# Optimization experiments

Hardware: AMD Instinct MI355X
Metric: run time of the kernel (lower is better)

The kernel has to match this reference:

```python
import jax, jax.numpy as jnp
import numpy as np

MODES = 256


def setup_inputs() -> dict:
    key = jax.random.key(0)
    k1, k2, k3, k4, k5 = jax.random.split(key, 5)
    B, C_IN, C_OUT, N, KM = 8, 128, 128, 8192, 32
    scale = 1.0 / (C_IN * C_OUT)
    return {
        "x": jax.random.normal(k1, (B, C_IN, N), dtype=jnp.float32),
        "wbases": jax.random.normal(k2, (B, N, MODES), dtype=jnp.float32),
        "bases": jax.random.normal(k3, (B, N, MODES), dtype=jnp.float32),
        "weights": scale * jax.random.normal(k4, (C_IN, C_OUT, KM), dtype=jnp.float32),
        "D": jax.random.normal(k5, (KM, MODES), dtype=jnp.float32),
    }


def reference(x, wbases, bases, weights, D):
    # Project onto weighted bases: (b, c_in, n) x (b, n, modes) -> (b, c_in, modes)
    x_hat = jnp.einsum('bcx,bxk->bck', x, wbases[:, :, :MODES])
    # D-weighted channel mixing. Original: x_hat1[b,i,j,k] = x_hat[b,i,k]*D[j,k];
    # y[b,o,k] = sum_{i,j} x_hat1[b,i,j,k] * weights[i,o,j]
    # Equivalent fused contraction (same math, no 4D broadcast):
    y_hat = jnp.einsum('bik,jk,ioj->bok', x_hat, D, weights)
    # Reconstruct on output bases: (b, c_out, modes) x (b, n, modes) -> (b, c_out, n)
    y = jnp.einsum('bck,bxk->bcx', y_hat, bases[:, :, :MODES])
    return y
```

## Files before the change

### kernel.cpp

```cpp
#include <hip/hip_runtime.h>

#define B_    8
#define CIN   128
#define COUT  128
#define NX    8192
#define KMJ   32
#define MODES 256

typedef short bf16x8 __attribute__((ext_vector_type(8)));
typedef float f32x4  __attribute__((ext_vector_type(4)));

__device__ __forceinline__ float bf2f(unsigned short u) {
    union { unsigned int i; float f; } v; v.i = ((unsigned int)u) << 16; return v.f;
}
__device__ __forceinline__ unsigned short f2bf(float f) {
    union { float f; unsigned int i; } v; v.f = f;
    unsigned int x = v.i;
    return (unsigned short)((x + 0x7fffu + ((x >> 16) & 1u)) >> 16);
}
__device__ __forceinline__ bf16x8 cvt8(const float* __restrict__ p) {
    f32x4 a = *(const f32x4*)p;
    f32x4 b = *(const f32x4*)(p + 4);
    bf16x8 r;
    r[0] = (short)f2bf(a[0]); r[1] = (short)f2bf(a[1]);
    r[2] = (short)f2bf(a[2]); r[3] = (short)f2bf(a[3]);
    r[4] = (short)f2bf(b[0]); r[5] = (short)f2bf(b[1]);
    r[6] = (short)f2bf(b[2]); r[7] = (short)f2bf(b[3]);
    return r;
}
__device__ __forceinline__ ushort4 cvt4(f32x4 a) {
    ushort4 r;
    r.x = f2bf(a[0]); r.y = f2bf(a[1]); r.z = f2bf(a[2]); r.w = f2bf(a[3]);
    return r;
}

__global__ __launch_bounds__(256) void k1_wk(const float* __restrict__ W,
                                             const float* __restrict__ D,
                                             unsigned short* __restrict__ Wk) {
    int wave = threadIdx.x >> 6;
    int lane = threadIdx.x & 63;
    int gw   = blockIdx.x * 4 + wave;
    int kt   = gw & 15;
    int ioch = gw >> 4;
    int k0   = kt * 16;
    int quad = lane >> 4, l16 = lane & 15;

    bf16x8 bfrag;
#pragma unroll
    for (int jj = 0; jj < 8; jj++)
        bfrag[jj] = (short)f2bf(D[(quad * 8 + jj) * MODES + k0 + l16]);

    int io0 = ioch * 256;
#pragma unroll 4
    for (int t = 0; t < 16; t++) {
        int io = io0 + t * 16 + l16;
        bf16x8 afrag = cvt8(W + (size_t)io * KMJ + quad * 8);
        f32x4 acc = {0.f, 0.f, 0.f, 0.f};
        acc = __builtin_amdgcn_mfma_f32_16x16x32_bf16(afrag, bfrag, acc, 0, 0, 0);
        int iorow = io0 + t * 16 + quad * 4;
        ushort4 st;
        st.x = f2bf(acc[0]); st.y = f2bf(acc[1]);
        st.z = f2bf(acc[2]); st.w = f2bf(acc[3]);
        *(ushort4*)(Wk + (size_t)(k0 + l16) * (CIN * COUT) + iorow) = st;
    }
}

__global__ __launch_bounds__(256) void k2_xhat(const float* __restrict__ X,
                                               const float* __restrict__ WB,
                                               float* __restrict__ XH) {
    __shared__ __align__(16) unsigned short Xs[128 * 40];
    __shared__ __align__(16) unsigned short WBs[32 * 140];
    int nt = blockIdx.x;
    int kt = blockIdx.y;
    int b  = blockIdx.z;
    int r0 = nt * 256;
    int t  = threadIdx.x;
    int wave = t >> 6, lane = t & 63;
    int wm = wave >> 1, wn = wave & 1;
    int quad = lane >> 4, l16 = lane & 15;

    const float* xb  = X  + (size_t)b * CIN * NX;
    const float* wbb = WB + (size_t)b * NX * MODES + kt * 128;

    int xn4 = t & 7,  xc0 = t >> 3;
    int wm4 = t & 31, wn0 = t >> 5;

    f32x4 acc[4][4];
#pragma unroll
    for (int i = 0; i < 4; i++)
#pragma unroll
        for (int j = 0; j < 4; j++) acc[i][j] = (f32x4){0.f, 0.f, 0.f, 0.f};

    for (int s = 0; s < 8; s++) {
        int rs = r0 + s * 32;
        f32x4 xv[4], wv[4];
#pragma unroll
        for (int r = 0; r < 4; r++)
            xv[r] = *(const f32x4*)(xb + (size_t)(xc0 + 32 * r) * NX + rs + xn4 * 4);
#pragma unroll
        for (int r = 0; r < 4; r++)
            wv[r] = *(const f32x4*)(wbb + (size_t)(rs + wn0 + 8 * r) * MODES + wm4 * 4);

        __syncthreads();
#pragma unroll
        for (int r = 0; r < 4; r++)
            *(ushort4*)(Xs + (xc0 + 32 * r) * 40 + xn4 * 4) = cvt4(xv[r]);
#pragma unroll
        for (int r = 0; r < 4; r++)
            *(ushort4*)(WBs + (wn0 + 8 * r) * 140 + wm4 * 4) = cvt4(wv[r]);
        __syncthreads();

        bf16x8 af[4];
#pragma unroll
        for (int tm = 0; tm < 4; tm++) {
            int c = wm * 64 + tm * 16 + l16;
            af[tm] = *(const bf16x8*)(Xs + c * 40 + quad * 8);
        }
        bf16x8 bfv[4];
#pragma unroll
        for (int tn = 0; tn < 4; tn++) {
            int km = wn * 64 + tn * 16 + l16;
#pragma unroll
            for (int jj = 0; jj < 8; jj++)
                bfv[tn][jj] = (short)WBs[(quad * 8 + jj) * 140 + km];
        }
#pragma unroll
        for (int tm = 0; tm < 4; tm++)
#pragma unroll
            for (int tn = 0; tn < 4; tn++)
                acc[tm][tn] = __builtin_amdgcn_mfma_f32_16x16x32_bf16(af[tm], bfv[tn], acc[tm][tn], 0, 0, 0);
    }

    float* xhb = XH + (size_t)b * CIN * MODES + kt * 128;
#pragma unroll
    for (int tm = 0; tm < 4; tm++) {
        int c = wm * 64 + tm * 16 + quad * 4;
#pragma unroll
        for (int tn = 0; tn < 4; tn++) {
            int km = wn * 64 + tn * 16 + l16;
#pragma unroll
            for (int r = 0; r < 4; r++)
                atomicAdd(xhb + (size_t)(c + r) * MODES + km, acc[tm][tn][r]);
        }
    }
}

__global__ __launch_bounds__(256) void k3_yhat(const float* __restrict__ XH,
                                               const unsigned short* __restrict__ Wk,
                                               unsigned short* __restrict__ YH) {
    __shared__ float xs[8][128];
    __shared__ float ys[8][128];
    int b  = blockIdx.y;
    int k0 = blockIdx.x * 8;
    int t  = threadIdx.x;
    const float* xhb = XH + (size_t)b * CIN * MODES;
#pragma unroll
    for (int l = 0; l < 4; l++) {
        int e = l * 256 + t;
        int kk = e & 7, i = e >> 3;
        xs[kk][i] = xhb[(size_t)i * MODES + k0 + kk];
    }
    __syncthreads();
    int o = t & 127, kh = t >> 7;
#pragma unroll
    for (int p = 0; p < 4; p++) {
        int kk = p * 2 + kh;
        int k  = k0 + kk;
        const unsigned short* wp = Wk + (size_t)k * (CIN * COUT) + o;
        float acc = 0.f;
#pragma unroll 8
        for (int i = 0; i < 128; i++)
            acc += xs[kk][i] * bf2f(wp[i * COUT]);
        ys[kk][o] = acc;
    }
    __syncthreads();
    unsigned short* yb = YH + (size_t)b * COUT * MODES;
#pragma unroll
    for (int l = 0; l < 4; l++) {
        int e = l * 256 + t;
        int kk = e & 7, oo = e >> 3;
        yb[(size_t)oo * MODES + k0 + kk] = f2bf(ys[kk][oo]);
    }
}

__global__ __launch_bounds__(256) void k4_y(const unsigned short* __restrict__ YH,
                                            const float* __restrict__ BA,
                                            float* __restrict__ Y) {
    __shared__ __align__(16) unsigned short As[128 * 32];
    __shared__ __align__(16) unsigned short Bs[128 * 32];
    int b  = blockIdx.y;
    int n0 = blockIdx.x * 128;
    int t  = threadIdx.x;
    int wave = t >> 6, lane = t & 63;
    int wm = wave >> 1, wn = wave & 1;
    int quad = lane >> 4, l16 = lane & 15;

    const unsigned short* yhb = YH + (size_t)b * COUT * MODES;
    const float* bab = BA + (size_t)b * NX * MODES + (size_t)n0 * MODES;

    f32x4 acc[4][4];
#pragma unroll
    for (int i = 0; i < 4; i++)
#pragma unroll
        for (int j = 0; j < 4; j++) acc[i][j] = (f32x4){0.f, 0.f, 0.f, 0.f};

    for (int step = 0; step < 8; step++) {
        int ks = step * 32;
#pragma unroll
        for (int p = 0; p < 2; p++) {
            int E = p * 2048 + t * 8;
            int row = E >> 5, kk = E & 31;
            bf16x8 av = *(const bf16x8*)(yhb + (size_t)row * MODES + ks + kk);
            bf16x8 bv = cvt8(bab + (size_t)row * MODES + ks + kk);
            *(bf16x8*)(As + E) = av;
            *(bf16x8*)(Bs + E) = bv;
        }
        __syncthreads();

        bf16x8 af[4], bfv[4];
#pragma unroll
        for (int tm = 0; tm < 4; tm++) {
            int c = wm * 64 + tm * 16 + l16;
            af[tm] = *(const bf16x8*)(As + c * 32 + quad * 8);
        }
#pragma unroll
        for (int tn = 0; tn < 4; tn++) {
            int n = wn * 64 + tn * 16 + l16;
            bfv[tn] = *(const bf16x8*)(Bs + n * 32 + quad * 8);
        }
#pragma unroll
        for (int tm = 0; tm < 4; tm++)
#pragma unroll
            for (int tn = 0; tn < 4; tn++)
                acc[tm][tn] = __builtin_amdgcn_mfma_f32_16x16x32_bf16(af[tm], bfv[tn], acc[tm][tn], 0, 0, 0);
        __syncthreads();
    }

    float* yb = Y + (size_t)b * COUT * NX;
#pragma unroll
    for (int tm = 0; tm < 4; tm++) {
        int o = wm * 64 + tm * 16 + quad * 4;
#pragma unroll
        for (int tn = 0; tn < 4; tn++) {
            int n = n0 + wn * 64 + tn * 16 + l16;
#pragma unroll
            for (int r = 0; r < 4; r++)
                yb[(size_t)(o + r) * NX + n] = acc[tm][tn][r];
        }
    }
}

extern "C" void kernel_launch(void* const* d_in, const int* in_sizes, int n_in,
                              void* d_out, int out_size, void* d_ws, size_t ws_size,
                              hipStream_t stream) {
    const float* X  = (const float*)d_in[0];
    const float* WB = (const float*)d_in[1];
    const float* BA = (const float*)d_in[2];
    const float* W  = (const float*)d_in[3];
    const float* D  = (const float*)d_in[4];
    float* Y = (float*)d_out;

    char* ws = (char*)d_ws;
    float*          XH = (float*)ws;
    unsigned short* Wk = (unsigned short*)(ws + (1u << 20));
    unsigned short* YH = (unsigned short*)(ws + (1u << 20) + (size_t)CIN * COUT * MODES * 2);

    hipMemsetAsync(XH, 0, (size_t)B_ * CIN * MODES * sizeof(float), stream);

    k1_wk  <<<256,            256, 0, stream>>>(W, D, Wk);
    k2_xhat<<<dim3(32, 2, 8), 256, 0, stream>>>(X, WB, XH);
    k3_yhat<<<dim3(32, 8),    256, 0, stream>>>(XH, Wk, YH);
    k4_y   <<<dim3(64, 8),    256, 0, stream>>>(YH, BA, Y);
}
```

Measured before the change: 251.1 us.

## Replace atomics with bf16 partials plus reduction, rework Wk layout and prefetch in k4

The x_hat kernel now uses 512-thread blocks covering all 256 modes and writes per-tile bf16 partial sums, which a new reduction kernel sums, replacing the float atomics and the memset. The Wk layout becomes [k][o][i], so k3 processes one mode across all batches with vectorized weight loads. k4 gains register prefetch of the next K-slice to overlap global loads with MFMA. The risks are extra partial-buffer traffic and bf16 rounding of the partial sums.

```diff
diff --git a/kernel.cpp b/kernel.cpp
--- a/kernel.cpp
+++ b/kernel.cpp
@@ -37,53 +37,43 @@
 __global__ __launch_bounds__(256) void k1_wk(const float* __restrict__ W,
                                              const float* __restrict__ D,
                                              unsigned short* __restrict__ Wk) {
-    int wave = threadIdx.x >> 6;
-    int lane = threadIdx.x & 63;
-    int gw   = blockIdx.x * 4 + wave;
-    int kt   = gw & 15;
-    int ioch = gw >> 4;
-    int k0   = kt * 16;
+    int wave = threadIdx.x >> 6, lane = threadIdx.x & 63;
     int quad = lane >> 4, l16 = lane & 15;
-
-    bf16x8 bfrag;
-#pragma unroll
-    for (int jj = 0; jj < 8; jj++)
-        bfrag[jj] = (short)f2bf(D[(quad * 8 + jj) * MODES + k0 + l16]);
-
-    int io0 = ioch * 256;
-#pragma unroll 4
-    for (int t = 0; t < 16; t++) {
-        int io = io0 + t * 16 + l16;
-        bf16x8 afrag = cvt8(W + (size_t)io * KMJ + quad * 8);
+    int gw  = blockIdx.x * 4 + wave;
+    int oi0 = gw * 16;
+    int i0  = oi0 & 127, o0 = oi0 >> 7;
+    bf16x8 bfrag = cvt8(W + ((size_t)(i0 + l16) * COUT + o0) * KMJ + quad * 8);
+    for (int mt = 0; mt < 16; mt++) {
+        int k0 = mt * 16;
+        bf16x8 afrag;
+#pragma unroll
+        for (int jj = 0; jj < 8; jj++)
+            afrag[jj] = (short)f2bf(D[(quad * 8 + jj) * MODES + k0 + l16]);
         f32x4 acc = {0.f, 0.f, 0.f, 0.f};
         acc = __builtin_amdgcn_mfma_f32_16x16x32_bf16(afrag, bfrag, acc, 0, 0, 0);
-        int iorow = io0 + t * 16 + quad * 4;
-        ushort4 st;
-        st.x = f2bf(acc[0]); st.y = f2bf(acc[1]);
-        st.z = f2bf(acc[2]); st.w = f2bf(acc[3]);
-        *(ushort4*)(Wk + (size_t)(k0 + l16) * (CIN * COUT) + iorow) = st;
-    }
-}
-
-__global__ __launch_bounds__(256) void k2_xhat(const float* __restrict__ X,
+#pragma unroll
+        for (int r = 0; r < 4; r++)
+            Wk[(size_t)(k0 + quad * 4 + r) * (CIN * COUT) + oi0 + l16] = f2bf(acc[r]);
+    }
+}
+
+__global__ __launch_bounds__(512) void k2_xhat(const float* __restrict__ X,
                                                const float* __restrict__ WB,
-                                               float* __restrict__ XH) {
+                                               unsigned short* __restrict__ PART) {
     __shared__ __align__(16) unsigned short Xs[128 * 40];
-    __shared__ __align__(16) unsigned short WBs[32 * 140];
-    int nt = blockIdx.x;
-    int kt = blockIdx.y;
-    int b  = blockIdx.z;
+    __shared__ __align__(16) unsigned short WBs[32 * 260];
+    int nt = blockIdx.x, b = blockIdx.y;
     int r0 = nt * 256;
     int t  = threadIdx.x;
     int wave = t >> 6, lane = t & 63;
-    int wm = wave >> 1, wn = wave & 1;
+    int wm = wave >> 2, wn = wave & 3;
     int quad = lane >> 4, l16 = lane & 15;
 
     const float* xb  = X  + (size_t)b * CIN * NX;
-    const float* wbb = WB + (size_t)b * NX * MODES + kt * 128;
-
-    int xn4 = t & 7,  xc0 = t >> 3;
-    int wm4 = t & 31, wn0 = t >> 5;
+    const float* wbb = WB + (size_t)b * NX * MODES;
+
+    int xn4 = t & 7,  xc  = t >> 3;
+    int wk4 = t & 63, wn0 = t >> 6;
 
     f32x4 acc[4][4];
 #pragma unroll
@@ -93,36 +83,32 @@
 
     for (int s = 0; s < 8; s++) {
         int rs = r0 + s * 32;
-        f32x4 xv[4], wv[4];
+        f32x4 xv0 = *(const f32x4*)(xb + (size_t)xc * NX + rs + xn4 * 4);
+        f32x4 xv1 = *(const f32x4*)(xb + (size_t)(xc + 64) * NX + rs + xn4 * 4);
+        f32x4 wv[4];
 #pragma unroll
         for (int r = 0; r < 4; r++)
-            xv[r] = *(const f32x4*)(xb + (size_t)(xc0 + 32 * r) * NX + rs + xn4 * 4);
+            wv[r] = *(const f32x4*)(wbb + (size_t)(rs + wn0 + 8 * r) * MODES + wk4 * 4);
+
+        __syncthreads();
+        *(ushort4*)(Xs + xc * 40 + xn4 * 4)        = cvt4(xv0);
+        *(ushort4*)(Xs + (xc + 64) * 40 + xn4 * 4) = cvt4(xv1);
 #pragma unroll
         for (int r = 0; r < 4; r++)
-            wv[r] = *(const f32x4*)(wbb + (size_t)(rs + wn0 + 8 * r) * MODES + wm4 * 4);
-
-        __syncthreads();
-#pragma unroll
-        for (int r = 0; r < 4; r++)
-            *(ushort4*)(Xs + (xc0 + 32 * r) * 40 + xn4 * 4) = cvt4(xv[r]);
-#pragma unroll
-        for (int r = 0; r < 4; r++)
-            *(ushort4*)(WBs + (wn0 + 8 * r) * 140 + wm4 * 4) = cvt4(wv[r]);
+            *(ushort4*)(WBs + (wn0 + 8 * r) * 260 + wk4 * 4) = cvt4(wv[r]);
         __syncthreads();
 
         bf16x8 af[4];
 #pragma unroll
-        for (int tm = 0; tm < 4; tm++) {
-            int c = wm * 64 + tm * 16 + l16;
-            af[tm] = *(const bf16x8*)(Xs + c * 40 + quad * 8);
-        }
+        for (int tm = 0; tm < 4; tm++)
+            af[tm] = *(const bf16x8*)(Xs + (wm * 64 + tm * 16 + l16) * 40 + quad * 8);
         bf16x8 bfv[4];
 #pragma unroll
         for (int tn = 0; tn < 4; tn++) {
             int km = wn * 64 + tn * 16 + l16;
 #pragma unroll
             for (int jj = 0; jj < 8; jj++)
-                bfv[tn][jj] = (short)WBs[(quad * 8 + jj) * 140 + km];
+                bfv[tn][jj] = (short)WBs[(quad * 8 + jj) * 260 + km];
         }
 #pragma unroll
         for (int tm = 0; tm < 4; tm++)
@@ -131,7 +117,7 @@
                 acc[tm][tn] = __builtin_amdgcn_mfma_f32_16x16x32_bf16(af[tm], bfv[tn], acc[tm][tn], 0, 0, 0);
     }
 
-    float* xhb = XH + (size_t)b * CIN * MODES + kt * 128;
+    unsigned short* pb = PART + ((size_t)b * 32 + nt) * (CIN * MODES);
 #pragma unroll
     for (int tm = 0; tm < 4; tm++) {
         int c = wm * 64 + tm * 16 + quad * 4;
@@ -140,47 +126,54 @@
             int km = wn * 64 + tn * 16 + l16;
 #pragma unroll
             for (int r = 0; r < 4; r++)
-                atomicAdd(xhb + (size_t)(c + r) * MODES + km, acc[tm][tn][r]);
-        }
+                pb[(size_t)(c + r) * MODES + km] = f2bf(acc[tm][tn][r]);
+        }
+    }
+}
+
+__global__ __launch_bounds__(256) void k2b_red(const unsigned short* __restrict__ PART,
+                                               float* __restrict__ XH) {
+    int e0 = blockIdx.x * 1024 + threadIdx.x;
+#pragma unroll
+    for (int r = 0; r < 4; r++) {
+        int e = e0 + r * 256;
+        int b = e >> 15, rem = e & 32767;
+        const unsigned short* p = PART + (size_t)b * 32 * (CIN * MODES) + rem;
+        float acc = 0.f;
+#pragma unroll
+        for (int nt = 0; nt < 32; nt++) acc += bf2f(p[nt * (CIN * MODES)]);
+        XH[e] = acc;
     }
 }
 
 __global__ __launch_bounds__(256) void k3_yhat(const float* __restrict__ XH,
                                                const unsigned short* __restrict__ Wk,
                                                unsigned short* __restrict__ YH) {
-    __shared__ float xs[8][128];
-    __shared__ float ys[8][128];
-    int b  = blockIdx.y;
-    int k0 = blockIdx.x * 8;
-    int t  = threadIdx.x;
-    const float* xhb = XH + (size_t)b * CIN * MODES;
+    __shared__ float xs[128][8];
+    int k = blockIdx.x;
+    int t = threadIdx.x;
 #pragma unroll
     for (int l = 0; l < 4; l++) {
         int e = l * 256 + t;
-        int kk = e & 7, i = e >> 3;
-        xs[kk][i] = xhb[(size_t)i * MODES + k0 + kk];
+        int i = e >> 3, b = e & 7;
+        xs[i][b] = XH[(size_t)b * (CIN * MODES) + (size_t)i * MODES + k];
     }
     __syncthreads();
-    int o = t & 127, kh = t >> 7;
-#pragma unroll
-    for (int p = 0; p < 4; p++) {
-        int kk = p * 2 + kh;
-        int k  = k0 + kk;
-        const unsigned short* wp = Wk + (size_t)k * (CIN * COUT) + o;
-        float acc = 0.f;
-#pragma unroll 8
-        for (int i = 0; i < 128; i++)
-            acc += xs[kk][i] * bf2f(wp[i * COUT]);
-        ys[kk][o] = acc;
-    }
-    __syncthreads();
-    unsigned short* yb = YH + (size_t)b * COUT * MODES;
-#pragma unroll
-    for (int l = 0; l < 4; l++) {
-        int e = l * 256 + t;
-        int kk = e & 7, oo = e >> 3;
-        yb[(size_t)oo * MODES + k0 + kk] = f2bf(ys[kk][oo]);
-    }
+    int o = t & 127, bh = t >> 7;
+    const unsigned short* wp = Wk + (size_t)k * (CIN * COUT) + (size_t)o * CIN;
+    f32x4 acc = {0.f, 0.f, 0.f, 0.f};
+    for (int ii = 0; ii < 16; ii++) {
+        bf16x8 wc = *(const bf16x8*)(wp + ii * 8);
+#pragma unroll
+        for (int jj = 0; jj < 8; jj++) {
+            float w = bf2f((unsigned short)wc[jj]);
+            f32x4 xv = *(const f32x4*)&xs[ii * 8 + jj][bh * 4];
+            acc += w * xv;
+        }
+    }
+#pragma unroll
+    for (int r = 0; r < 4; r++)
+        YH[((size_t)(bh * 4 + r) * COUT + o) * MODES + k] = f2bf(acc[r]);
 }
 
 __global__ __launch_bounds__(256) void k4_y(const unsigned short* __restrict__ YH,
@@ -198,24 +191,49 @@
     const unsigned short* yhb = YH + (size_t)b * COUT * MODES;
     const float* bab = BA + (size_t)b * NX * MODES + (size_t)n0 * MODES;
 
+    int E0 = t * 8;
+    int row0 = E0 >> 5, kk0 = E0 & 31;
+    int row1 = (2048 + E0) >> 5, kk1 = (2048 + E0) & 31;
+
     f32x4 acc[4][4];
 #pragma unroll
     for (int i = 0; i < 4; i++)
 #pragma unroll
         for (int j = 0; j < 4; j++) acc[i][j] = (f32x4){0.f, 0.f, 0.f, 0.f};
 
+    bf16x8 av0 = *(const bf16x8*)(yhb + (size_t)row0 * MODES + kk0);
+    bf16x8 av1 = *(const bf16x8*)(yhb + (size_t)row1 * MODES + kk1);
+    f32x4 bv0a = *(const f32x4*)(bab + (size_t)row0 * MODES + kk0);
+    f32x4 bv0b = *(const f32x4*)(bab + (size_t)row0 * MODES + kk0 + 4);
+    f32x4 bv1a = *(const f32x4*)(bab + (size_t)row1 * MODES + kk1);
+    f32x4 bv1b = *(const f32x4*)(bab + (size_t)row1 * MODES + kk1 + 4);
+
     for (int step = 0; step < 8; step++) {
-        int ks = step * 32;
-#pragma unroll
-        for (int p = 0; p < 2; p++) {
-            int E = p * 2048 + t * 8;
-            int row = E >> 5, kk = E & 31;
-            bf16x8 av = *(const bf16x8*)(yhb + (size_t)row * MODES + ks + kk);
-            bf16x8 bv = cvt8(bab + (size_t)row * MODES + ks + kk);
-            *(bf16x8*)(As + E) = av;
-            *(bf16x8*)(Bs + E) = bv;
-        }
-        __syncthreads();
+        __syncthreads();
+        *(bf16x8*)(As + E0)        = av0;
+        *(bf16x8*)(As + 2048 + E0) = av1;
+        bf16x8 bs0, bs1;
+        bs0[0]=(short)f2bf(bv0a[0]); bs0[1]=(short)f2bf(bv0a[1]);
+        bs0[2]=(short)f2bf(bv0a[2]); bs0[3]=(short)f2bf(bv0a[3]);
+        bs0[4]=(short)f2bf(bv0b[0]); bs0[5]=(short)f2bf(bv0b[1]);
+        bs0[6]=(short)f2bf(bv0b[2]); bs0[7]=(short)f2bf(bv0b[3]);
+        bs1[0]=(short)f2bf(bv1a[0]); bs1[1]=(short)f2bf(bv1a[1]);
+        bs1[2]=(short)f2bf(bv1a[2]); bs1[3]=(short)f2bf(bv1a[3]);
+        bs1[4]=(short)f2bf(bv1b[0]); bs1[5]=(short)f2bf(bv1b[1]);
+        bs1[6]=(short)f2bf(bv1b[2]); bs1[7]=(short)f2bf(bv1b[3]);
+        *(bf16x8*)(Bs + E0)        = bs0;
+        *(bf16x8*)(Bs + 2048 + E0) = bs1;
+        __syncthreads();
+
+        if (step < 7) {
+            int ks = (step + 1) * 32;
+            av0  = *(const bf16x8*)(yhb + (size_t)row0 * MODES + ks + kk0);
+            av1  = *(const bf16x8*)(yhb + (size_t)row1 * MODES + ks + kk1);
+            bv0a = *(const f32x4*)(bab + (size_t)row0 * MODES + ks + kk0);
+            bv0b = *(const f32x4*)(bab + (size_t)row0 * MODES + ks + kk0 + 4);
+            bv1a = *(const f32x4*)(bab + (size_t)row1 * MODES + ks + kk1);
+            bv1b = *(const f32x4*)(bab + (size_t)row1 * MODES + ks + kk1 + 4);
+        }
 
         bf16x8 af[4], bfv[4];
 #pragma unroll
@@ -233,7 +251,6 @@
 #pragma unroll
             for (int tn = 0; tn < 4; tn++)
                 acc[tm][tn] = __builtin_amdgcn_mfma_f32_16x16x32_bf16(af[tm], bfv[tn], acc[tm][tn], 0, 0, 0);
-        __syncthreads();
     }
 
     float* yb = Y + (size_t)b * COUT * NX;
@@ -261,14 +278,14 @@
     float* Y = (float*)d_out;
 
     char* ws = (char*)d_ws;
-    float*          XH = (float*)ws;
-    unsigned short* Wk = (unsigned short*)(ws + (1u << 20));
-    unsigned short* YH = (unsigned short*)(ws + (1u << 20) + (size_t)CIN * COUT * MODES * 2);
-
-    hipMemsetAsync(XH, 0, (size_t)B_ * CIN * MODES * sizeof(float), stream);
-
-    k1_wk  <<<256,            256, 0, stream>>>(W, D, Wk);
-    k2_xhat<<<dim3(32, 2, 8), 256, 0, stream>>>(X, WB, XH);
-    k3_yhat<<<dim3(32, 8),    256, 0, stream>>>(XH, Wk, YH);
-    k4_y   <<<dim3(64, 8),    256, 0, stream>>>(YH, BA, Y);
-}
+    unsigned short* Wk   = (unsigned short*)ws;
+    float*          XH   = (float*)(ws + (8u << 20));
+    unsigned short* YH   = (unsigned short*)(ws + (9u << 20));
+    unsigned short* PART = (unsigned short*)(ws + (10u << 20));
+
+    k1_wk  <<<256,          256, 0, stream>>>(W, D, Wk);
+    k2_xhat<<<dim3(32, 8),  512, 0, stream>>>(X, WB, PART);
+    k2b_red<<<256,          256, 0, stream>>>(PART, XH);
+    k3_yhat<<<MODES,        256, 0, stream>>>(XH, Wk, YH);
+    k4_y   <<<dim3(64, 8),  256, 0, stream>>>(YH, BA, Y);
+}
```

Result: faster. 220.3 us (-12.3%).
